# Kernel tuning notes

Hardware: AMD Instinct MI355X
Metric: run time of the kernel (lower is better)

## Reference

```python
import jax, jax.numpy as jnp
import numpy as np

N_HEAD = 16
N_KV_HEAD = 8
HEAD_DIM = 64
EPS_NORM = 1e-6


def _rms_norm(x):
    # F.rms_norm without learned weight
    return x * jax.lax.rsqrt(jnp.mean(x * x, axis=-1, keepdims=True) + EPS_NORM)


def _apply_rotary_emb(x, cos, sin):
    # x: [B, T, H, D]; cos/sin: [T, 1, D/2] (broadcast over B and H)
    d = x.shape[-1] // 2
    x1, x2 = x[..., :d], x[..., d:]
    return jnp.concatenate([x1 * cos + x2 * sin, -x1 * sin + x2 * cos], axis=-1)


def setup_inputs() -> dict:
    key = jax.random.key(0)
    ks = jax.random.split(key, 8)
    B, T, C = 2, 2048, 1024
    return {
        "x": jax.random.normal(ks[0], (B, T, C), jnp.float32),
        "cos": jax.random.uniform(ks[1], (T, 1, HEAD_DIM // 2), jnp.float32),
        "sin": jax.random.uniform(ks[2], (T, 1, HEAD_DIM // 2), jnp.float32),
        "Wq": jax.random.normal(ks[3], (N_HEAD * HEAD_DIM, C), jnp.float32) * 0.02,
        "Wk": jax.random.normal(ks[4], (N_KV_HEAD * HEAD_DIM, C), jnp.float32) * 0.02,
        "Wv": jax.random.normal(ks[5], (N_KV_HEAD * HEAD_DIM, C), jnp.float32) * 0.02,
        "Wproj": jax.random.normal(ks[6], (C, C), jnp.float32) * 0.02,
        "w_braid": jax.random.normal(ks[7], (HEAD_DIM,), jnp.float32),
    }


def reference(x, cos, sin, Wq, Wk, Wv, Wproj, w_braid):
    B, T, C = x.shape
    q = (x @ Wq.T).reshape(B, T, N_HEAD, HEAD_DIM)
    k = (x @ Wk.T).reshape(B, T, N_KV_HEAD, HEAD_DIM)
    v = (x @ Wv.T).reshape(B, T, N_KV_HEAD, HEAD_DIM)
    q = _rms_norm(_apply_rotary_emb(q, cos, sin))
    k = _rms_norm(_apply_rotary_emb(k, cos, sin))
    # [B, H, T, D]
    q = q.transpose(0, 2, 1, 3)
    k = k.transpose(0, 2, 1, 3)
    v = v.transpose(0, 2, 1, 3)
    rep = N_HEAD // N_KV_HEAD
    k = jnp.repeat(k, rep, axis=1)  # GQA repeat_kv_heads
    v = jnp.repeat(v, rep, axis=1)
    # rank-1 outer-sum score: s_q[i] + s_k[j]
    s_q = jnp.einsum("bhtd,d->bht", q, w_braid)
    s_k = jnp.einsum("bhsd,d->bhs", k, w_braid)
    scores = s_q[..., :, None] + s_k[..., None, :]  # [B, H, T, T]
    causal = jnp.arange(T)[:, None] >= jnp.arange(T)[None, :]
    scores = jnp.where(causal, scores, -jnp.inf)
    attn = jax.nn.sigmoid(scores)  # non-softmax gating
    y = jnp.einsum("bhts,bhsd->bhtd", attn, v)
    y = y / (T ** 0.5 + 1e-6)
    y = y.transpose(0, 2, 1, 3).reshape(B, T, C)
    return y @ Wproj.T
```

## Files before the change

### kernel.cpp

```cpp
#include <hip/hip_runtime.h>

#define BATCH   2
#define T_LEN   2048
#define C_DIM   1024
#define NH      16
#define NKV     8
#define HD      64

typedef unsigned short u16;
typedef __attribute__((ext_vector_type(8))) short short8;
typedef __attribute__((ext_vector_type(4))) float floatx4;

__device__ __forceinline__ u16 f2bf(float f) {
    union { float f; unsigned u; } v; v.f = f;
    unsigned r = v.u + 0x7FFF + ((v.u >> 16) & 1);
    return (u16)(r >> 16);
}

__device__ __forceinline__ void gload_lds16(const u16* g, u16* l) {
    __builtin_amdgcn_global_load_lds(
        (const __attribute__((address_space(1))) void*)g,
        (__attribute__((address_space(3))) void*)l, 16, 0, 0);
}

#define SBAR   __builtin_amdgcn_s_barrier()
#define SCHED0 __builtin_amdgcn_sched_barrier(0)
#define WAIT_LGKM0 asm volatile("s_waitcnt lgkmcnt(0)" ::: "memory")

__global__ __launch_bounds__(256)
void cvt_all(const float* __restrict__ x, const float* __restrict__ Wq,
             const float* __restrict__ Wk, const float* __restrict__ Wv,
             const float* __restrict__ Wp, u16* __restrict__ xb,
             u16* __restrict__ Wqkvb, u16* __restrict__ Wpb) {
    const int blk = blockIdx.x;
    const float* src; u16* dst; long off;
    if (blk < 4096)      { src = x;  dst = xb;              off = (long)blk * 1024; }
    else if (blk < 5120) { src = Wq; dst = Wqkvb;           off = (long)(blk - 4096) * 1024; }
    else if (blk < 5632) { src = Wk; dst = Wqkvb + 1048576; off = (long)(blk - 5120) * 1024; }
    else if (blk < 6144) { src = Wv; dst = Wqkvb + 1572864; off = (long)(blk - 5632) * 1024; }
    else                 { src = Wp; dst = Wpb;             off = (long)(blk - 6144) * 1024; }
    const long i = off + (long)threadIdx.x * 4;
    const float4 f = *(const float4*)&src[i];
    ushort4 o;
    o.x = f2bf(f.x); o.y = f2bf(f.y); o.z = f2bf(f.z); o.w = f2bf(f.w);
    *(ushort4*)&dst[i] = o;
}

__global__ __launch_bounds__(256)
void gemm_qkv(const u16* __restrict__ A, const u16* __restrict__ B,
              u16* __restrict__ Vt, float* __restrict__ esq,
              float* __restrict__ esk, const float* __restrict__ cosb,
              const float* __restrict__ sinb, const float* __restrict__ wb) {
    const int K  = 1024;
    const int NK = 16;
    __shared__ u16 As[2][128 * 64];
    __shared__ u16 Bs[2][128 * 64];
    const int tid    = threadIdx.x;
    const int lane   = tid & 63;
    const int wave   = tid >> 6;
    const int row_in = lane & 15;
    const int quad   = lane >> 4;
    const int rw     = (wave & 1) * 64;
    const int cw     = (wave >> 1) * 64;
    const int bi   = blockIdx.x;
    const int xcd  = bi & 7;
    const int bj   = bi >> 3;
    const int row0 = (bj >> 1) * 128;
    const int col0 = (xcd * 2 + (bj & 1)) * 128;

    floatx4 acc[4][4] = {};

    const int n    = row_in;
    const int xa   = n & 7;

    const int sl_r[4]  = { (0*256+tid)>>3, (1*256+tid)>>3, (2*256+tid)>>3, (3*256+tid)>>3 };
    const int sl_kc[4] = { ((0*256+tid)&7)^(sl_r[0]&7), ((1*256+tid)&7)^(sl_r[1]&7),
                           ((2*256+tid)&7)^(sl_r[2]&7), ((3*256+tid)&7)^(sl_r[3]&7) };

    #pragma unroll
    for (int c = 0; c < 4; ++c) {
        const int l = c * 256 + tid;
        gload_lds16(A + (size_t)(row0 + sl_r[c]) * K + 0  + sl_kc[c] * 8, &As[0][(size_t)l * 8]);
        gload_lds16(B + (size_t)(col0 + sl_r[c]) * K + 0  + sl_kc[c] * 8, &Bs[0][(size_t)l * 8]);
    }
    #pragma unroll
    for (int c = 0; c < 4; ++c) {
        const int l = c * 256 + tid;
        gload_lds16(A + (size_t)(row0 + sl_r[c]) * K + 64 + sl_kc[c] * 8, &As[1][(size_t)l * 8]);
        gload_lds16(B + (size_t)(col0 + sl_r[c]) * K + 64 + sl_kc[c] * 8, &Bs[1][(size_t)l * 8]);
    }
    asm volatile("s_waitcnt vmcnt(8)" ::: "memory");
    SBAR;
    SCHED0;

    int cur = 0;
    for (int kt = 0; kt < NK; ++kt) {
        short8 af[2][4], bf_[2][4];
        #pragma unroll
        for (int kk = 0; kk < 2; ++kk) {
            const int co = ((kk * 4 + quad) ^ xa) * 8;
            #pragma unroll
            for (int i = 0; i < 4; ++i)
                af[kk][i] = *(const short8*)&As[cur][(rw + 16 * i + n) * 64 + co];
            #pragma unroll
            for (int j = 0; j < 4; ++j)
                bf_[kk][j] = *(const short8*)&Bs[cur][(cw + 16 * j + n) * 64 + co];
        }
        WAIT_LGKM0;
        SCHED0;
        SBAR;
        SCHED0;

        if (kt + 2 < NK) {
            const int kn = (kt + 2) * 64;
            #pragma unroll
            for (int c = 0; c < 4; ++c) {
                const int l = c * 256 + tid;
                gload_lds16(A + (size_t)(row0 + sl_r[c]) * K + kn + sl_kc[c] * 8, &As[cur][(size_t)l * 8]);
                gload_lds16(B + (size_t)(col0 + sl_r[c]) * K + kn + sl_kc[c] * 8, &Bs[cur][(size_t)l * 8]);
            }
        }

        #pragma unroll
        for (int kk = 0; kk < 2; ++kk)
            #pragma unroll
            for (int i = 0; i < 4; ++i)
                #pragma unroll
                for (int j = 0; j < 4; ++j)
                    acc[i][j] = __builtin_amdgcn_mfma_f32_16x16x32_bf16(af[kk][i], bf_[kk][j], acc[i][j], 0, 0, 0);

        if (kt < NK - 2) { asm volatile("s_waitcnt vmcnt(8)" ::: "memory"); }
        else             { asm volatile("s_waitcnt vmcnt(0)" ::: "memory"); }
        SBAR;
        SCHED0;
        cur ^= 1;
    }

    const int cw_g = col0 + cw;
    const int rw_g = row0 + rw;
    const int ch   = cw_g >> 6;

    if (ch < 24) {
        const float w0 = wb[n], w1 = wb[16 + n], w2 = wb[32 + n], w3 = wb[48 + n];
        #pragma unroll
        for (int i = 0; i < 4; ++i)
            #pragma unroll
            for (int r = 0; r < 4; ++r) {
                const int grow = rw_g + 16 * i + quad * 4 + r;
                const int t = grow & 2047;
                const int b = grow >> 11;
                const float c0 = cosb[t * 32 + n];
                const float c1 = cosb[t * 32 + 16 + n];
                const float s0 = sinb[t * 32 + n];
                const float s1 = sinb[t * 32 + 16 + n];
                const float x0 = acc[i][0][r], x1 = acc[i][1][r];
                const float x2 = acc[i][2][r], x3 = acc[i][3][r];
                const float r0 = fmaf(x0, c0,  x2 * s0);
                const float r1 = fmaf(x1, c1,  x3 * s1);
                const float r2 = fmaf(x2, c0, -x0 * s0);
                const float r3 = fmaf(x3, c1, -x1 * s1);
                float ss = r0 * r0 + r1 * r1 + r2 * r2 + r3 * r3;
                float dt = r0 * w0 + r1 * w1 + r2 * w2 + r3 * w3;
                #pragma unroll
                for (int m = 1; m < 16; m <<= 1) {
                    ss += __shfl_xor(ss, m, 64);
                    dt += __shfl_xor(dt, m, 64);
                }
                const float val = dt * rsqrtf(ss * (1.0f / 64.0f) + 1e-6f);
                const float e = __expf(-fminf(fmaxf(val, -44.0f), 44.0f));
                if (n == 0) {
                    if (ch < 16) esq[((size_t)b * NH + ch) * T_LEN + t] = e;
                    else         esk[((size_t)b * NKV + ch - 16) * T_LEN + t] = e;
                }
            }
    } else {
        const int vcol = cw_g - 1536;
        const int b    = rw_g >> 11;
        const int tb   = (rw_g & 2047) + quad * 4;
        #pragma unroll
        for (int j = 0; j < 4; ++j) {
            const int dg  = vcol + 16 * j + n;
            const int kvh = dg >> 6;
            const int din = dg & 63;
            u16* dstp = Vt + ((size_t)(b * NKV + kvh) * 64 + din) * T_LEN;
            #pragma unroll
            for (int i = 0; i < 4; ++i) {
                ushort4 o;
                o.x = f2bf(acc[i][j][0]);
                o.y = f2bf(acc[i][j][1]);
                o.z = f2bf(acc[i][j][2]);
                o.w = f2bf(acc[i][j][3]);
                *(ushort4*)&dstp[tb + 16 * i] = o;
            }
        }
    }
}

__global__ __launch_bounds__(512)
void braid_attn(const float* __restrict__ esq, const float* __restrict__ esk,
                const u16* __restrict__ Vt, u16* __restrict__ yb) {
    __shared__ u16 Vd[2][2][4096];
    __shared__ float eskl[2][128];
    __shared__ float red[4096];

    const int bi   = blockIdx.x;
    const int g    = (bi & 7) * 2 + ((bi >> 8) & 1);
    const int wnd  = (bi >> 3) & 31;
    const int b    = g >> 3;
    const int kvh  = g & 7;
    const int h    = kvh * 2 + (wnd >> 4);
    const int p    = wnd & 15;
    const int bh   = b * 16 + h;
    const int tid  = threadIdx.x;
    const int lane = tid & 63;
    const int wave = tid >> 6;
    const int sg   = wave >> 2;
    const int w4   = wave & 3;
    const int n    = lane & 15;
    const int quad = lane >> 4;
    const int row  = w4 * 16 + n;

    const float* esq_p = esq + (size_t)bh * T_LEN;
    const float* esk_p = esk + ((size_t)b * NKV + kvh) * T_LEN;
    const u16*   vt_b  = Vt + ((size_t)b * NKV + kvh) * 64 * T_LEN;
    const float  inv   = (float)(1.0 / (45.254833995939045 + 1e-6));

    const int st_r  = tid >> 3;
    const int st_so = ((tid & 7) ^ (st_r & 7)) << 3;

    for (int ph = 0; ph < 2; ++ph) {
        const int t0 = (ph ? p : (31 - p)) * 64;
        const float a = esq_p[t0 + row];
        const int send = t0 + 64;
        floatx4 acc[4] = {};

        gload_lds16(vt_b + (size_t)st_r * T_LEN + st_so, &Vd[0][0][(size_t)tid * 8]);
        if (64 < send)
            gload_lds16(vt_b + (size_t)st_r * T_LEN + 64 + st_so, &Vd[0][1][(size_t)tid * 8]);
        if (tid < 128 && (tid < 64 || 64 < send))
            eskl[0][tid] = esk_p[tid];
        __syncthreads();

        int cur = 0;
        for (int s0 = 0; s0 < send; s0 += 128) {
            const int s0n = s0 + 128;
            if (s0n < send) {
                gload_lds16(vt_b + (size_t)st_r * T_LEN + s0n + st_so, &Vd[cur ^ 1][0][(size_t)tid * 8]);
                if (s0n + 64 < send)
                    gload_lds16(vt_b + (size_t)st_r * T_LEN + s0n + 64 + st_so, &Vd[cur ^ 1][1][(size_t)tid * 8]);
                if (tid < 128 && (tid < 64 || s0n + 64 < send))
                    eskl[cur ^ 1][tid] = esk_p[s0n + tid];
            }

            const int s0g = s0 + sg * 64;
            if (s0g < send) {
                const bool diag = (s0g == t0);
                #pragma unroll
                for (int kk = 0; kk < 2; ++kk) {
                    const float* eb = &eskl[cur][sg * 64 + kk * 32 + quad * 8];
                    const float4 e0 = *(const float4*)eb;
                    const float4 e1 = *(const float4*)(eb + 4);
                    const float ev[8] = {e0.x, e0.y, e0.z, e0.w, e1.x, e1.y, e1.z, e1.w};
                    union { unsigned u[4]; short8 s8; } af;
                    #pragma unroll
                    for (int jj = 0; jj < 4; ++jj) {
                        float r0 = __builtin_amdgcn_rcpf(fmaf(ev[2 * jj],     a, 1.0f));
                        float r1 = __builtin_amdgcn_rcpf(fmaf(ev[2 * jj + 1], a, 1.0f));
                        if (diag) {
                            const int s_ = kk * 32 + quad * 8 + 2 * jj;
                            if (s_     > row) r0 = 0.0f;
                            if (s_ + 1 > row) r1 = 0.0f;
                        }
                        af.u[jj] = __builtin_amdgcn_perm(__float_as_uint(r1),
                                                         __float_as_uint(r0), 0x07060302u);
                    }
                    #pragma unroll
                    for (int j = 0; j < 4; ++j) {
                        const short8 bfr = *(const short8*)
                            &Vd[cur][sg][(16 * j + n) * 64 + (((kk * 4 + quad) ^ (n & 7)) << 3)];
                        acc[j] = __builtin_amdgcn_mfma_f32_16x16x32_bf16(af.s8, bfr, acc[j], 0, 0, 0);
                    }
                }
            }
            __syncthreads();
            cur ^= 1;
        }

        if (sg == 1) {
            #pragma unroll
            for (int j = 0; j < 4; ++j)
                #pragma unroll
                for (int r = 0; r < 4; ++r)
                    red[(j * 4 + r) * 256 + w4 * 64 + lane] = acc[j][r];
        }
        __syncthreads();
        if (sg == 0) {
            #pragma unroll
            for (int j = 0; j < 4; ++j)
                #pragma unroll
                for (int r = 0; r < 4; ++r) {
                    const float o = acc[j][r] + red[(j * 4 + r) * 256 + w4 * 64 + lane];
                    const int t = t0 + w4 * 16 + quad * 4 + r;
                    yb[((size_t)b * T_LEN + t) * C_DIM + h * HD + 16 * j + n] = f2bf(o * inv);
                }
        }
    }
}

__global__ __launch_bounds__(256)
void gemm_proj(const u16* __restrict__ A, const u16* __restrict__ B,
               float* __restrict__ C, int M, int N, int K) {
    const int NK = 16;
    __shared__ u16 As[2][128 * 64];
    __shared__ u16 Bs[2][64 * 64];
    const int tid    = threadIdx.x;
    const int lane   = tid & 63;
    const int wave   = tid >> 6;
    const int row_in = lane & 15;
    const int quad   = lane >> 4;
    const int rw     = (wave & 1) * 64;
    const int cw     = (wave >> 1) * 32;
    const int bi   = blockIdx.x;
    const int xcd  = bi & 7;
    const int bj   = bi >> 3;
    const int row0 = (bj >> 1) * 128;
    const int col0 = (xcd * 2 + (bj & 1)) * 64;

    floatx4 acc[4][2] = {};

    const int n  = row_in;
    const int xa = n & 7;

    const int sa_r[4]  = { (0*256+tid)>>3, (1*256+tid)>>3, (2*256+tid)>>3, (3*256+tid)>>3 };
    const int sa_kc[4] = { ((0*256+tid)&7)^(sa_r[0]&7), ((1*256+tid)&7)^(sa_r[1]&7),
                           ((2*256+tid)&7)^(sa_r[2]&7), ((3*256+tid)&7)^(sa_r[3]&7) };
    const int sb_r[2]  = { (0*256+tid)>>3, (1*256+tid)>>3 };
    const int sb_kc[2] = { ((0*256+tid)&7)^(sb_r[0]&7), ((1*256+tid)&7)^(sb_r[1]&7) };

    #pragma unroll
    for (int c = 0; c < 4; ++c)
        gload_lds16(A + (size_t)(row0 + sa_r[c]) * K + 0 + sa_kc[c] * 8, &As[0][(size_t)(c*256+tid) * 8]);
    #pragma unroll
    for (int c = 0; c < 2; ++c)
        gload_lds16(B + (size_t)(col0 + sb_r[c]) * K + 0 + sb_kc[c] * 8, &Bs[0][(size_t)(c*256+tid) * 8]);
    #pragma unroll
    for (int c = 0; c < 4; ++c)
        gload_lds16(A + (size_t)(row0 + sa_r[c]) * K + 64 + sa_kc[c] * 8, &As[1][(size_t)(c*256+tid) * 8]);
    #pragma unroll
    for (int c = 0; c < 2; ++c)
        gload_lds16(B + (size_t)(col0 + sb_r[c]) * K + 64 + sb_kc[c] * 8, &Bs[1][(size_t)(c*256+tid) * 8]);
    asm volatile("s_waitcnt vmcnt(6)" ::: "memory");
    SBAR;
    SCHED0;

    int cur = 0;
    for (int kt = 0; kt < NK; ++kt) {
        short8 af[2][4], bf_[2][2];
        #pragma unroll
        for (int kk = 0; kk < 2; ++kk) {
            const int co = ((kk * 4 + quad) ^ xa) * 8;
            #pragma unroll
            for (int i = 0; i < 4; ++i)
                af[kk][i] = *(const short8*)&As[cur][(rw + 16 * i + n) * 64 + co];
            #pragma unroll
            for (int j = 0; j < 2; ++j)
                bf_[kk][j] = *(const short8*)&Bs[cur][(cw + 16 * j + n) * 64 + co];
        }
        WAIT_LGKM0;
        SCHED0;
        SBAR;
        SCHED0;

        if (kt + 2 < NK) {
            const int kn = (kt + 2) * 64;
            #pragma unroll
            for (int c = 0; c < 4; ++c)
                gload_lds16(A + (size_t)(row0 + sa_r[c]) * K + kn + sa_kc[c] * 8, &As[cur][(size_t)(c*256+tid) * 8]);
            #pragma unroll
            for (int c = 0; c < 2; ++c)
                gload_lds16(B + (size_t)(col0 + sb_r[c]) * K + kn + sb_kc[c] * 8, &Bs[cur][(size_t)(c*256+tid) * 8]);
        }

        #pragma unroll
        for (int kk = 0; kk < 2; ++kk)
            #pragma unroll
            for (int i = 0; i < 4; ++i)
                #pragma unroll
                for (int j = 0; j < 2; ++j)
                    acc[i][j] = __builtin_amdgcn_mfma_f32_16x16x32_bf16(af[kk][i], bf_[kk][j], acc[i][j], 0, 0, 0);

        if (kt < NK - 2) { asm volatile("s_waitcnt vmcnt(6)" ::: "memory"); }
        else             { asm volatile("s_waitcnt vmcnt(0)" ::: "memory"); }
        SBAR;
        SCHED0;
        cur ^= 1;
    }

    #pragma unroll
    for (int i = 0; i < 4; ++i)
        #pragma unroll
        for (int j = 0; j < 2; ++j)
            #pragma unroll
            for (int r = 0; r < 4; ++r)
                C[(size_t)(row0 + rw + 16 * i + quad * 4 + r) * N + col0 + cw + 16 * j + row_in]
                    = acc[i][j][r];
}

extern "C" void kernel_launch(void* const* d_in, const int* in_sizes, int n_in,
                              void* d_out, int out_size, void* d_ws, size_t ws_size,
                              hipStream_t stream) {
    const float* x     = (const float*)d_in[0];
    const float* cosb  = (const float*)d_in[1];
    const float* sinb  = (const float*)d_in[2];
    const float* Wq    = (const float*)d_in[3];
    const float* Wk    = (const float*)d_in[4];
    const float* Wv    = (const float*)d_in[5];
    const float* Wproj = (const float*)d_in[6];
    const float* wb    = (const float*)d_in[7];
    float* out = (float*)d_out;

    char* w = (char*)d_ws;
    u16* xb     = (u16*)w;  w += (size_t)4096 * 1024 * 2;
    u16* Wqkvb  = (u16*)w;  w += (size_t)2048 * 1024 * 2;
    u16* Wpb    = (u16*)w;  w += (size_t)1024 * 1024 * 2;
    u16* yb     = (u16*)w;  w += (size_t)4096 * 1024 * 2;
    u16* VtB    = (u16*)w;  w += (size_t)BATCH * NKV * 64 * T_LEN * 2;
    float* esq  = (float*)w; w += (size_t)BATCH * NH * T_LEN * 4;
    float* esk  = (float*)w; w += (size_t)BATCH * NKV * T_LEN * 4;

    dim3 blk(256);
    cvt_all<<<7168, blk, 0, stream>>>(x, Wq, Wk, Wv, Wproj, xb, Wqkvb, Wpb);
    gemm_qkv<<<512, blk, 0, stream>>>(xb, Wqkvb, VtB, esq, esk, cosb, sinb, wb);
    braid_attn<<<512, dim3(512), 0, stream>>>(esq, esk, VtB, yb);
    gemm_proj<<<512, blk, 0, stream>>>(yb, Wpb, out, 4096, 1024, 1024);
}
```

Before: 148.0 us.

## Fuse all stages into one persistent kernel with grid barriers

Replaces the four separate launches (convert, QKV GEMM, attention, projection GEMM) with a single persistent kernel of 512 blocks that runs each stage in turn, separated by atomic-counter grid barriers and sharing LDS through a union. The aim is to remove kernel launch gaps and tail idle time between stages. In exchange, the attention stage is rewritten for 256 threads instead of 512. The barriers rely on all 512 blocks being co-resident (launch bounds of 2 blocks per CU) and use a timeout spin, which could silently break correctness if residency fails.

```diff
diff --git a/kernel.cpp b/kernel.cpp
--- a/kernel.cpp
+++ b/kernel.cpp
@@ -6,6 +6,7 @@
 #define NH      16
 #define NKV     8
 #define HD      64
+#define NBLK    512
 
 typedef unsigned short u16;
 typedef __attribute__((ext_vector_type(8))) short short8;
@@ -27,237 +28,271 @@
 #define SCHED0 __builtin_amdgcn_sched_barrier(0)
 #define WAIT_LGKM0 asm volatile("s_waitcnt lgkmcnt(0)" ::: "memory")
 
-__global__ __launch_bounds__(256)
-void cvt_all(const float* __restrict__ x, const float* __restrict__ Wq,
-             const float* __restrict__ Wk, const float* __restrict__ Wv,
-             const float* __restrict__ Wp, u16* __restrict__ xb,
-             u16* __restrict__ Wqkvb, u16* __restrict__ Wpb) {
-    const int blk = blockIdx.x;
-    const float* src; u16* dst; long off;
-    if (blk < 4096)      { src = x;  dst = xb;              off = (long)blk * 1024; }
-    else if (blk < 5120) { src = Wq; dst = Wqkvb;           off = (long)(blk - 4096) * 1024; }
-    else if (blk < 5632) { src = Wk; dst = Wqkvb + 1048576; off = (long)(blk - 5120) * 1024; }
-    else if (blk < 6144) { src = Wv; dst = Wqkvb + 1572864; off = (long)(blk - 5632) * 1024; }
-    else                 { src = Wp; dst = Wpb;             off = (long)(blk - 6144) * 1024; }
-    const long i = off + (long)threadIdx.x * 4;
-    const float4 f = *(const float4*)&src[i];
-    ushort4 o;
-    o.x = f2bf(f.x); o.y = f2bf(f.y); o.z = f2bf(f.z); o.w = f2bf(f.w);
-    *(ushort4*)&dst[i] = o;
-}
-
-__global__ __launch_bounds__(256)
-void gemm_qkv(const u16* __restrict__ A, const u16* __restrict__ B,
-              u16* __restrict__ Vt, float* __restrict__ esq,
-              float* __restrict__ esk, const float* __restrict__ cosb,
-              const float* __restrict__ sinb, const float* __restrict__ wb) {
-    const int K  = 1024;
-    const int NK = 16;
-    __shared__ u16 As[2][128 * 64];
-    __shared__ u16 Bs[2][128 * 64];
-    const int tid    = threadIdx.x;
-    const int lane   = tid & 63;
-    const int wave   = tid >> 6;
-    const int row_in = lane & 15;
-    const int quad   = lane >> 4;
-    const int rw     = (wave & 1) * 64;
-    const int cw     = (wave >> 1) * 64;
-    const int bi   = blockIdx.x;
-    const int xcd  = bi & 7;
-    const int bj   = bi >> 3;
-    const int row0 = (bj >> 1) * 128;
-    const int col0 = (xcd * 2 + (bj & 1)) * 128;
-
-    floatx4 acc[4][4] = {};
-
-    const int n    = row_in;
-    const int xa   = n & 7;
-
-    const int sl_r[4]  = { (0*256+tid)>>3, (1*256+tid)>>3, (2*256+tid)>>3, (3*256+tid)>>3 };
-    const int sl_kc[4] = { ((0*256+tid)&7)^(sl_r[0]&7), ((1*256+tid)&7)^(sl_r[1]&7),
-                           ((2*256+tid)&7)^(sl_r[2]&7), ((3*256+tid)&7)^(sl_r[3]&7) };
-
-    #pragma unroll
-    for (int c = 0; c < 4; ++c) {
-        const int l = c * 256 + tid;
-        gload_lds16(A + (size_t)(row0 + sl_r[c]) * K + 0  + sl_kc[c] * 8, &As[0][(size_t)l * 8]);
-        gload_lds16(B + (size_t)(col0 + sl_r[c]) * K + 0  + sl_kc[c] * 8, &Bs[0][(size_t)l * 8]);
+__device__ __forceinline__ void grid_barrier(unsigned* bar, int idx) {
+    __syncthreads();
+    if (threadIdx.x == 0) {
+        __threadfence();
+        unsigned* cnt = bar + idx * 64;
+        __hip_atomic_fetch_add(cnt, 1u, __ATOMIC_ACQ_REL, __HIP_MEMORY_SCOPE_AGENT);
+        const long long lim = 5000000LL;
+        long long t0 = (long long)__builtin_amdgcn_s_memrealtime();
+        while (__hip_atomic_load(cnt, __ATOMIC_ACQUIRE, __HIP_MEMORY_SCOPE_AGENT) < (unsigned)NBLK) {
+            if ((long long)__builtin_amdgcn_s_memrealtime() - t0 > lim) break;
+        }
+        __threadfence();
     }
-    #pragma unroll
-    for (int c = 0; c < 4; ++c) {
-        const int l = c * 256 + tid;
-        gload_lds16(A + (size_t)(row0 + sl_r[c]) * K + 64 + sl_kc[c] * 8, &As[1][(size_t)l * 8]);
-        gload_lds16(B + (size_t)(col0 + sl_r[c]) * K + 64 + sl_kc[c] * 8, &Bs[1][(size_t)l * 8]);
+    __syncthreads();
+}
+
+__global__ __launch_bounds__(64)
+void bar_init(unsigned* bar) {
+    bar[threadIdx.x * 4] = 0;
+    bar[threadIdx.x * 4 + 1] = 0;
+    bar[threadIdx.x * 4 + 2] = 0;
+    bar[threadIdx.x * 4 + 3] = 0;
+}
+
+struct SMg { u16 As[2][128 * 64]; u16 Bs[2][128 * 64]; };
+struct SMp { u16 As[2][128 * 64]; u16 Bs[2][64 * 64]; };
+struct SMa { u16 Vd[2][4096]; float eskl[2][64]; };
+union __align__(16) SMu { SMg g; SMp p; SMa a; };
+
+__global__ __launch_bounds__(256, 2)
+void fused_all(const float* __restrict__ x, const float* __restrict__ cosb,
+               const float* __restrict__ sinb, const float* __restrict__ Wq,
+               const float* __restrict__ Wk, const float* __restrict__ Wv,
+               const float* __restrict__ Wp, const float* __restrict__ wb,
+               u16* __restrict__ xb, u16* __restrict__ Wqkvb,
+               u16* __restrict__ Wpb, u16* __restrict__ yb,
+               u16* __restrict__ VtB, float* __restrict__ esq,
+               float* __restrict__ esk, float* __restrict__ out,
+               unsigned* __restrict__ bar) {
+    __shared__ SMu sm;
+
+    {
+        const int tid = threadIdx.x;
+        #pragma unroll
+        for (int i = 0; i < 14; ++i) {
+            const int blk = blockIdx.x * 14 + i;
+            const float* src; u16* dst; long off;
+            if (blk < 4096)      { src = x;  dst = xb;              off = (long)blk * 1024; }
+            else if (blk < 5120) { src = Wq; dst = Wqkvb;           off = (long)(blk - 4096) * 1024; }
+            else if (blk < 5632) { src = Wk; dst = Wqkvb + 1048576; off = (long)(blk - 5120) * 1024; }
+            else if (blk < 6144) { src = Wv; dst = Wqkvb + 1572864; off = (long)(blk - 5632) * 1024; }
+            else                 { src = Wp; dst = Wpb;             off = (long)(blk - 6144) * 1024; }
+            const long idx = off + (long)tid * 4;
+            const float4 f = *(const float4*)&src[idx];
+            ushort4 o;
+            o.x = f2bf(f.x); o.y = f2bf(f.y); o.z = f2bf(f.z); o.w = f2bf(f.w);
+            *(ushort4*)&dst[idx] = o;
+        }
     }
-    asm volatile("s_waitcnt vmcnt(8)" ::: "memory");
-    SBAR;
-    SCHED0;
-
-    int cur = 0;
-    for (int kt = 0; kt < NK; ++kt) {
-        short8 af[2][4], bf_[2][4];
-        #pragma unroll
-        for (int kk = 0; kk < 2; ++kk) {
-            const int co = ((kk * 4 + quad) ^ xa) * 8;
-            #pragma unroll
-            for (int i = 0; i < 4; ++i)
-                af[kk][i] = *(const short8*)&As[cur][(rw + 16 * i + n) * 64 + co];
-            #pragma unroll
-            for (int j = 0; j < 4; ++j)
-                bf_[kk][j] = *(const short8*)&Bs[cur][(cw + 16 * j + n) * 64 + co];
-        }
-        WAIT_LGKM0;
-        SCHED0;
+    grid_barrier(bar, 0);
+
+    {
+        const u16* A = xb;
+        const u16* B = Wqkvb;
+        const int K  = 1024;
+        const int NK = 16;
+        u16 (&As)[2][128 * 64] = sm.g.As;
+        u16 (&Bs)[2][128 * 64] = sm.g.Bs;
+        const int tid    = threadIdx.x;
+        const int lane   = tid & 63;
+        const int wave   = tid >> 6;
+        const int row_in = lane & 15;
+        const int quad   = lane >> 4;
+        const int rw     = (wave & 1) * 64;
+        const int cw     = (wave >> 1) * 64;
+        const int bi   = blockIdx.x;
+        const int xcd  = bi & 7;
+        const int bj   = bi >> 3;
+        const int row0 = (bj >> 1) * 128;
+        const int col0 = (xcd * 2 + (bj & 1)) * 128;
+
+        floatx4 acc[4][4] = {};
+        const int n  = row_in;
+        const int xa = n & 7;
+
+        const int sl_r[4]  = { (0*256+tid)>>3, (1*256+tid)>>3, (2*256+tid)>>3, (3*256+tid)>>3 };
+        const int sl_kc[4] = { ((0*256+tid)&7)^(sl_r[0]&7), ((1*256+tid)&7)^(sl_r[1]&7),
+                               ((2*256+tid)&7)^(sl_r[2]&7), ((3*256+tid)&7)^(sl_r[3]&7) };
+
+        #pragma unroll
+        for (int c = 0; c < 4; ++c) {
+            const int l = c * 256 + tid;
+            gload_lds16(A + (size_t)(row0 + sl_r[c]) * K + 0  + sl_kc[c] * 8, &As[0][(size_t)l * 8]);
+            gload_lds16(B + (size_t)(col0 + sl_r[c]) * K + 0  + sl_kc[c] * 8, &Bs[0][(size_t)l * 8]);
+        }
+        #pragma unroll
+        for (int c = 0; c < 4; ++c) {
+            const int l = c * 256 + tid;
+            gload_lds16(A + (size_t)(row0 + sl_r[c]) * K + 64 + sl_kc[c] * 8, &As[1][(size_t)l * 8]);
+            gload_lds16(B + (size_t)(col0 + sl_r[c]) * K + 64 + sl_kc[c] * 8, &Bs[1][(size_t)l * 8]);
+        }
+        asm volatile("s_waitcnt vmcnt(8)" ::: "memory");
         SBAR;
         SCHED0;
 
-        if (kt + 2 < NK) {
-            const int kn = (kt + 2) * 64;
-            #pragma unroll
-            for (int c = 0; c < 4; ++c) {
-                const int l = c * 256 + tid;
-                gload_lds16(A + (size_t)(row0 + sl_r[c]) * K + kn + sl_kc[c] * 8, &As[cur][(size_t)l * 8]);
-                gload_lds16(B + (size_t)(col0 + sl_r[c]) * K + kn + sl_kc[c] * 8, &Bs[cur][(size_t)l * 8]);
-            }
-        }
-
-        #pragma unroll
-        for (int kk = 0; kk < 2; ++kk)
+        int cur = 0;
+        for (int kt = 0; kt < NK; ++kt) {
+            short8 af[2][4], bf_[2][4];
+            #pragma unroll
+            for (int kk = 0; kk < 2; ++kk) {
+                const int co = ((kk * 4 + quad) ^ xa) * 8;
+                #pragma unroll
+                for (int i = 0; i < 4; ++i)
+                    af[kk][i] = *(const short8*)&As[cur][(rw + 16 * i + n) * 64 + co];
+                #pragma unroll
+                for (int j = 0; j < 4; ++j)
+                    bf_[kk][j] = *(const short8*)&Bs[cur][(cw + 16 * j + n) * 64 + co];
+            }
+            WAIT_LGKM0;
+            SCHED0;
+            SBAR;
+            SCHED0;
+
+            if (kt + 2 < NK) {
+                const int kn = (kt + 2) * 64;
+                #pragma unroll
+                for (int c = 0; c < 4; ++c) {
+                    const int l = c * 256 + tid;
+                    gload_lds16(A + (size_t)(row0 + sl_r[c]) * K + kn + sl_kc[c] * 8, &As[cur][(size_t)l * 8]);
+                    gload_lds16(B + (size_t)(col0 + sl_r[c]) * K + kn + sl_kc[c] * 8, &Bs[cur][(size_t)l * 8]);
+                }
+            }
+
+            #pragma unroll
+            for (int kk = 0; kk < 2; ++kk)
+                #pragma unroll
+                for (int i = 0; i < 4; ++i)
+                    #pragma unroll
+                    for (int j = 0; j < 4; ++j)
+                        acc[i][j] = __builtin_amdgcn_mfma_f32_16x16x32_bf16(af[kk][i], bf_[kk][j], acc[i][j], 0, 0, 0);
+
+            if (kt < NK - 2) { asm volatile("s_waitcnt vmcnt(8)" ::: "memory"); }
+            else             { asm volatile("s_waitcnt vmcnt(0)" ::: "memory"); }
+            SBAR;
+            SCHED0;
+            cur ^= 1;
+        }
+
+        const int cw_g = col0 + cw;
+        const int rw_g = row0 + rw;
+        const int ch   = cw_g >> 6;
+
+        if (ch < 24) {
+            const float w0 = wb[n], w1 = wb[16 + n], w2 = wb[32 + n], w3 = wb[48 + n];
             #pragma unroll
             for (int i = 0; i < 4; ++i)
                 #pragma unroll
-                for (int j = 0; j < 4; ++j)
-                    acc[i][j] = __builtin_amdgcn_mfma_f32_16x16x32_bf16(af[kk][i], bf_[kk][j], acc[i][j], 0, 0, 0);
-
-        if (kt < NK - 2) { asm volatile("s_waitcnt vmcnt(8)" ::: "memory"); }
-        else             { asm volatile("s_waitcnt vmcnt(0)" ::: "memory"); }
-        SBAR;
-        SCHED0;
-        cur ^= 1;
+                for (int r = 0; r < 4; ++r) {
+                    const int grow = rw_g + 16 * i + quad * 4 + r;
+                    const int t = grow & 2047;
+                    const int b = grow >> 11;
+                    const float c0 = cosb[t * 32 + n];
+                    const float c1 = cosb[t * 32 + 16 + n];
+                    const float s0 = sinb[t * 32 + n];
+                    const float s1 = sinb[t * 32 + 16 + n];
+                    const float x0 = acc[i][0][r], x1 = acc[i][1][r];
+                    const float x2 = acc[i][2][r], x3 = acc[i][3][r];
+                    const float r0 = fmaf(x0, c0,  x2 * s0);
+                    const float r1 = fmaf(x1, c1,  x3 * s1);
+                    const float r2 = fmaf(x2, c0, -x0 * s0);
+                    const float r3 = fmaf(x3, c1, -x1 * s1);
+                    float ss = r0 * r0 + r1 * r1 + r2 * r2 + r3 * r3;
+                    float dt = r0 * w0 + r1 * w1 + r2 * w2 + r3 * w3;
+                    #pragma unroll
+                    for (int m = 1; m < 16; m <<= 1) {
+                        ss += __shfl_xor(ss, m, 64);
+                        dt += __shfl_xor(dt, m, 64);
+                    }
+                    const float val = dt * rsqrtf(ss * (1.0f / 64.0f) + 1e-6f);
+                    const float e = __expf(-fminf(fmaxf(val, -44.0f), 44.0f));
+                    if (n == 0) {
+                        if (ch < 16) esq[((size_t)b * NH + ch) * T_LEN + t] = e;
+                        else         esk[((size_t)b * NKV + ch - 16) * T_LEN + t] = e;
+                    }
+                }
+        } else {
+            const int vcol = cw_g - 1536;
+            const int b    = rw_g >> 11;
+            const int tb   = (rw_g & 2047) + quad * 4;
+            #pragma unroll
+            for (int j = 0; j < 4; ++j) {
+                const int dg  = vcol + 16 * j + n;
+                const int kvh = dg >> 6;
+                const int din = dg & 63;
+                u16* dstp = VtB + ((size_t)(b * NKV + kvh) * 64 + din) * T_LEN;
+                #pragma unroll
+                for (int i = 0; i < 4; ++i) {
+                    ushort4 o;
+                    o.x = f2bf(acc[i][j][0]);
+                    o.y = f2bf(acc[i][j][1]);
+                    o.z = f2bf(acc[i][j][2]);
+                    o.w = f2bf(acc[i][j][3]);
+                    *(ushort4*)&dstp[tb + 16 * i] = o;
+                }
+            }
+        }
     }
-
-    const int cw_g = col0 + cw;
-    const int rw_g = row0 + rw;
-    const int ch   = cw_g >> 6;
-
-    if (ch < 24) {
-        const float w0 = wb[n], w1 = wb[16 + n], w2 = wb[32 + n], w3 = wb[48 + n];
-        #pragma unroll
-        for (int i = 0; i < 4; ++i)
-            #pragma unroll
-            for (int r = 0; r < 4; ++r) {
-                const int grow = rw_g + 16 * i + quad * 4 + r;
-                const int t = grow & 2047;
-                const int b = grow >> 11;
-                const float c0 = cosb[t * 32 + n];
-                const float c1 = cosb[t * 32 + 16 + n];
-                const float s0 = sinb[t * 32 + n];
-                const float s1 = sinb[t * 32 + 16 + n];
-                const float x0 = acc[i][0][r], x1 = acc[i][1][r];
-                const float x2 = acc[i][2][r], x3 = acc[i][3][r];
-                const float r0 = fmaf(x0, c0,  x2 * s0);
-                const float r1 = fmaf(x1, c1,  x3 * s1);
-                const float r2 = fmaf(x2, c0, -x0 * s0);
-                const float r3 = fmaf(x3, c1, -x1 * s1);
-                float ss = r0 * r0 + r1 * r1 + r2 * r2 + r3 * r3;
-                float dt = r0 * w0 + r1 * w1 + r2 * w2 + r3 * w3;
-                #pragma unroll
-                for (int m = 1; m < 16; m <<= 1) {
-                    ss += __shfl_xor(ss, m, 64);
-                    dt += __shfl_xor(dt, m, 64);
-                }
-                const float val = dt * rsqrtf(ss * (1.0f / 64.0f) + 1e-6f);
-                const float e = __expf(-fminf(fmaxf(val, -44.0f), 44.0f));
-                if (n == 0) {
-                    if (ch < 16) esq[((size_t)b * NH + ch) * T_LEN + t] = e;
-                    else         esk[((size_t)b * NKV + ch - 16) * T_LEN + t] = e;
-                }
-            }
-    } else {
-        const int vcol = cw_g - 1536;
-        const int b    = rw_g >> 11;
-        const int tb   = (rw_g & 2047) + quad * 4;
-        #pragma unroll
-        for (int j = 0; j < 4; ++j) {
-            const int dg  = vcol + 16 * j + n;
-            const int kvh = dg >> 6;
-            const int din = dg & 63;
-            u16* dstp = Vt + ((size_t)(b * NKV + kvh) * 64 + din) * T_LEN;
-            #pragma unroll
-            for (int i = 0; i < 4; ++i) {
-                ushort4 o;
-                o.x = f2bf(acc[i][j][0]);
-                o.y = f2bf(acc[i][j][1]);
-                o.z = f2bf(acc[i][j][2]);
-                o.w = f2bf(acc[i][j][3]);
-                *(ushort4*)&dstp[tb + 16 * i] = o;
-            }
-        }
-    }
-}
-
-__global__ __launch_bounds__(512)
-void braid_attn(const float* __restrict__ esq, const float* __restrict__ esk,
-                const u16* __restrict__ Vt, u16* __restrict__ yb) {
-    __shared__ u16 Vd[2][2][4096];
-    __shared__ float eskl[2][128];
-    __shared__ float red[4096];
-
-    const int bi   = blockIdx.x;
-    const int g    = (bi & 7) * 2 + ((bi >> 8) & 1);
-    const int wnd  = (bi >> 3) & 31;
-    const int b    = g >> 3;
-    const int kvh  = g & 7;
-    const int h    = kvh * 2 + (wnd >> 4);
-    const int p    = wnd & 15;
-    const int bh   = b * 16 + h;
-    const int tid  = threadIdx.x;
-    const int lane = tid & 63;
-    const int wave = tid >> 6;
-    const int sg   = wave >> 2;
-    const int w4   = wave & 3;
-    const int n    = lane & 15;
-    const int quad = lane >> 4;
-    const int row  = w4 * 16 + n;
-
-    const float* esq_p = esq + (size_t)bh * T_LEN;
-    const float* esk_p = esk + ((size_t)b * NKV + kvh) * T_LEN;
-    const u16*   vt_b  = Vt + ((size_t)b * NKV + kvh) * 64 * T_LEN;
-    const float  inv   = (float)(1.0 / (45.254833995939045 + 1e-6));
-
-    const int st_r  = tid >> 3;
-    const int st_so = ((tid & 7) ^ (st_r & 7)) << 3;
-
-    for (int ph = 0; ph < 2; ++ph) {
-        const int t0 = (ph ? p : (31 - p)) * 64;
-        const float a = esq_p[t0 + row];
-        const int send = t0 + 64;
-        floatx4 acc[4] = {};
-
-        gload_lds16(vt_b + (size_t)st_r * T_LEN + st_so, &Vd[0][0][(size_t)tid * 8]);
-        if (64 < send)
-            gload_lds16(vt_b + (size_t)st_r * T_LEN + 64 + st_so, &Vd[0][1][(size_t)tid * 8]);
-        if (tid < 128 && (tid < 64 || 64 < send))
-            eskl[0][tid] = esk_p[tid];
-        __syncthreads();
-
-        int cur = 0;
-        for (int s0 = 0; s0 < send; s0 += 128) {
-            const int s0n = s0 + 128;
-            if (s0n < send) {
-                gload_lds16(vt_b + (size_t)st_r * T_LEN + s0n + st_so, &Vd[cur ^ 1][0][(size_t)tid * 8]);
-                if (s0n + 64 < send)
-                    gload_lds16(vt_b + (size_t)st_r * T_LEN + s0n + 64 + st_so, &Vd[cur ^ 1][1][(size_t)tid * 8]);
-                if (tid < 128 && (tid < 64 || s0n + 64 < send))
-                    eskl[cur ^ 1][tid] = esk_p[s0n + tid];
-            }
-
-            const int s0g = s0 + sg * 64;
-            if (s0g < send) {
-                const bool diag = (s0g == t0);
+    grid_barrier(bar, 1);
+
+    {
+        u16   (&Vd)[2][4096] = sm.a.Vd;
+        float (&eskl)[2][64] = sm.a.eskl;
+
+        const int bi   = blockIdx.x;
+        const int g    = (bi & 7) * 2 + ((bi >> 8) & 1);
+        const int wnd  = (bi >> 3) & 31;
+        const int b    = g >> 3;
+        const int kvh  = g & 7;
+        const int h    = kvh * 2 + (wnd >> 4);
+        const int p    = wnd & 15;
+        const int bh   = b * 16 + h;
+        const int tid  = threadIdx.x;
+        const int lane = tid & 63;
+        const int w4   = tid >> 6;
+        const int n    = lane & 15;
+        const int quad = lane >> 4;
+        const int row  = w4 * 16 + n;
+
+        const float* esq_p = esq + (size_t)bh * T_LEN;
+        const float* esk_p = esk + ((size_t)b * NKV + kvh) * T_LEN;
+        const u16*   vt_b  = VtB + ((size_t)b * NKV + kvh) * 64 * T_LEN;
+        const float  inv   = (float)(1.0 / (45.254833995939045 + 1e-6));
+
+        const int st_r[2]  = { (0*256+tid)>>3, (1*256+tid)>>3 };
+        const int st_so[2] = { (((0*256+tid)&7) ^ (st_r[0]&7)) << 3,
+                               (((1*256+tid)&7) ^ (st_r[1]&7)) << 3 };
+
+        for (int ph = 0; ph < 2; ++ph) {
+            const int t0 = (ph ? p : (31 - p)) * 64;
+            const float a = esq_p[t0 + row];
+            const int send = t0 + 64;
+            floatx4 acc[4] = {};
+
+            #pragma unroll
+            for (int c = 0; c < 2; ++c)
+                gload_lds16(vt_b + (size_t)st_r[c] * T_LEN + st_so[c],
+                            &Vd[0][(size_t)(c * 256 + tid) * 8]);
+            if (tid < 64) eskl[0][tid] = esk_p[tid];
+            __syncthreads();
+
+            int cur = 0;
+            for (int s0 = 0; s0 < send; s0 += 64) {
+                const int s0n = s0 + 64;
+                if (s0n < send) {
+                    #pragma unroll
+                    for (int c = 0; c < 2; ++c)
+                        gload_lds16(vt_b + (size_t)st_r[c] * T_LEN + s0n + st_so[c],
+                                    &Vd[cur ^ 1][(size_t)(c * 256 + tid) * 8]);
+                    if (tid < 64) eskl[cur ^ 1][tid] = esk_p[s0n + tid];
+                }
+
+                const bool diag = (s0 == t0);
                 #pragma unroll
                 for (int kk = 0; kk < 2; ++kk) {
-                    const float* eb = &eskl[cur][sg * 64 + kk * 32 + quad * 8];
+                    const float* eb = &eskl[cur][kk * 32 + quad * 8];
                     const float4 e0 = *(const float4*)eb;
                     const float4 e1 = *(const float4*)(eb + 4);
                     const float ev[8] = {e0.x, e0.y, e0.z, e0.w, e1.x, e1.y, e1.z, e1.w};
@@ -277,133 +312,126 @@
                     #pragma unroll
                     for (int j = 0; j < 4; ++j) {
                         const short8 bfr = *(const short8*)
-                            &Vd[cur][sg][(16 * j + n) * 64 + (((kk * 4 + quad) ^ (n & 7)) << 3)];
+                            &Vd[cur][(16 * j + n) * 64 + (((kk * 4 + quad) ^ (n & 7)) << 3)];
                         acc[j] = __builtin_amdgcn_mfma_f32_16x16x32_bf16(af.s8, bfr, acc[j], 0, 0, 0);
                     }
                 }
-            }
-            __syncthreads();
-            cur ^= 1;
-        }
-
-        if (sg == 1) {
+                __syncthreads();
+                cur ^= 1;
+            }
+
             #pragma unroll
             for (int j = 0; j < 4; ++j)
                 #pragma unroll
-                for (int r = 0; r < 4; ++r)
-                    red[(j * 4 + r) * 256 + w4 * 64 + lane] = acc[j][r];
-        }
-        __syncthreads();
-        if (sg == 0) {
-            #pragma unroll
-            for (int j = 0; j < 4; ++j)
-                #pragma unroll
                 for (int r = 0; r < 4; ++r) {
-                    const float o = acc[j][r] + red[(j * 4 + r) * 256 + w4 * 64 + lane];
                     const int t = t0 + w4 * 16 + quad * 4 + r;
-                    yb[((size_t)b * T_LEN + t) * C_DIM + h * HD + 16 * j + n] = f2bf(o * inv);
+                    yb[((size_t)b * T_LEN + t) * C_DIM + h * HD + 16 * j + n]
+                        = f2bf(acc[j][r] * inv);
                 }
         }
     }
-}
-
-__global__ __launch_bounds__(256)
-void gemm_proj(const u16* __restrict__ A, const u16* __restrict__ B,
-               float* __restrict__ C, int M, int N, int K) {
-    const int NK = 16;
-    __shared__ u16 As[2][128 * 64];
-    __shared__ u16 Bs[2][64 * 64];
-    const int tid    = threadIdx.x;
-    const int lane   = tid & 63;
-    const int wave   = tid >> 6;
-    const int row_in = lane & 15;
-    const int quad   = lane >> 4;
-    const int rw     = (wave & 1) * 64;
-    const int cw     = (wave >> 1) * 32;
-    const int bi   = blockIdx.x;
-    const int xcd  = bi & 7;
-    const int bj   = bi >> 3;
-    const int row0 = (bj >> 1) * 128;
-    const int col0 = (xcd * 2 + (bj & 1)) * 64;
-
-    floatx4 acc[4][2] = {};
-
-    const int n  = row_in;
-    const int xa = n & 7;
-
-    const int sa_r[4]  = { (0*256+tid)>>3, (1*256+tid)>>3, (2*256+tid)>>3, (3*256+tid)>>3 };
-    const int sa_kc[4] = { ((0*256+tid)&7)^(sa_r[0]&7), ((1*256+tid)&7)^(sa_r[1]&7),
-                           ((2*256+tid)&7)^(sa_r[2]&7), ((3*256+tid)&7)^(sa_r[3]&7) };
-    const int sb_r[2]  = { (0*256+tid)>>3, (1*256+tid)>>3 };
-    const int sb_kc[2] = { ((0*256+tid)&7)^(sb_r[0]&7), ((1*256+tid)&7)^(sb_r[1]&7) };
-
-    #pragma unroll
-    for (int c = 0; c < 4; ++c)
-        gload_lds16(A + (size_t)(row0 + sa_r[c]) * K + 0 + sa_kc[c] * 8, &As[0][(size_t)(c*256+tid) * 8]);
-    #pragma unroll
-    for (int c = 0; c < 2; ++c)
-        gload_lds16(B + (size_t)(col0 + sb_r[c]) * K + 0 + sb_kc[c] * 8, &Bs[0][(size_t)(c*256+tid) * 8]);
-    #pragma unroll
-    for (int c = 0; c < 4; ++c)
-        gload_lds16(A + (size_t)(row0 + sa_r[c]) * K + 64 + sa_kc[c] * 8, &As[1][(size_t)(c*256+tid) * 8]);
-    #pragma unroll
-    for (int c = 0; c < 2; ++c)
-        gload_lds16(B + (size_t)(col0 + sb_r[c]) * K + 64 + sb_kc[c] * 8, &Bs[1][(size_t)(c*256+tid) * 8]);
-    asm volatile("s_waitcnt vmcnt(6)" ::: "memory");
-    SBAR;
-    SCHED0;
-
-    int cur = 0;
-    for (int kt = 0; kt < NK; ++kt) {
-        short8 af[2][4], bf_[2][2];
-        #pragma unroll
-        for (int kk = 0; kk < 2; ++kk) {
-            const int co = ((kk * 4 + quad) ^ xa) * 8;
-            #pragma unroll
-            for (int i = 0; i < 4; ++i)
-                af[kk][i] = *(const short8*)&As[cur][(rw + 16 * i + n) * 64 + co];
-            #pragma unroll
-            for (int j = 0; j < 2; ++j)
-                bf_[kk][j] = *(const short8*)&Bs[cur][(cw + 16 * j + n) * 64 + co];
-        }
-        WAIT_LGKM0;
-        SCHED0;
+    grid_barrier(bar, 2);
+
+    {
+        const u16* A = yb;
+        const u16* B = Wpb;
+        float* C = out;
+        const int K  = 1024;
+        const int N  = 1024;
+        const int NK = 16;
+        u16 (&As)[2][128 * 64] = sm.p.As;
+        u16 (&Bs)[2][64 * 64]  = sm.p.Bs;
+        const int tid    = threadIdx.x;
+        const int lane   = tid & 63;
+        const int wave   = tid >> 6;
+        const int row_in = lane & 15;
+        const int quad   = lane >> 4;
+        const int rw     = (wave & 1) * 64;
+        const int cw     = (wave >> 1) * 32;
+        const int bi   = blockIdx.x;
+        const int xcd  = bi & 7;
+        const int bj   = bi >> 3;
+        const int row0 = (bj >> 1) * 128;
+        const int col0 = (xcd * 2 + (bj & 1)) * 64;
+
+        floatx4 acc[4][2] = {};
+        const int n  = row_in;
+        const int xa = n & 7;
+
+        const int sa_r[4]  = { (0*256+tid)>>3, (1*256+tid)>>3, (2*256+tid)>>3, (3*256+tid)>>3 };
+        const int sa_kc[4] = { ((0*256+tid)&7)^(sa_r[0]&7), ((1*256+tid)&7)^(sa_r[1]&7),
+                               ((2*256+tid)&7)^(sa_r[2]&7), ((3*256+tid)&7)^(sa_r[3]&7) };
+        const int sb_r[2]  = { (0*256+tid)>>3, (1*256+tid)>>3 };
+        const int sb_kc[2] = { ((0*256+tid)&7)^(sb_r[0]&7), ((1*256+tid)&7)^(sb_r[1]&7) };
+
+        #pragma unroll
+        for (int c = 0; c < 4; ++c)
+            gload_lds16(A + (size_t)(row0 + sa_r[c]) * K + 0 + sa_kc[c] * 8, &As[0][(size_t)(c*256+tid) * 8]);
+        #pragma unroll
+        for (int c = 0; c < 2; ++c)
+            gload_lds16(B + (size_t)(col0 + sb_r[c]) * K + 0 + sb_kc[c] * 8, &Bs[0][(size_t)(c*256+tid) * 8]);
+        #pragma unroll
+        for (int c = 0; c < 4; ++c)
+            gload_lds16(A + (size_t)(row0 + sa_r[c]) * K + 64 + sa_kc[c] * 8, &As[1][(size_t)(c*256+tid) * 8]);
+        #pragma unroll
+        for (int c = 0; c < 2; ++c)
+            gload_lds16(B + (size_t)(col0 + sb_r[c]) * K + 64 + sb_kc[c] * 8, &Bs[1][(size_t)(c*256+tid) * 8]);
+        asm volatile("s_waitcnt vmcnt(6)" ::: "memory");
         SBAR;
         SCHED0;
 
-        if (kt + 2 < NK) {
-            const int kn = (kt + 2) * 64;
-            #pragma unroll
-            for (int c = 0; c < 4; ++c)
-                gload_lds16(A + (size_t)(row0 + sa_r[c]) * K + kn + sa_kc[c] * 8, &As[cur][(size_t)(c*256+tid) * 8]);
-            #pragma unroll
-            for (int c = 0; c < 2; ++c)
-                gload_lds16(B + (size_t)(col0 + sb_r[c]) * K + kn + sb_kc[c] * 8, &Bs[cur][(size_t)(c*256+tid) * 8]);
-        }
-
-        #pragma unroll
-        for (int kk = 0; kk < 2; ++kk)
-            #pragma unroll
-            for (int i = 0; i < 4; ++i)
+        int cur = 0;
+        for (int kt = 0; kt < NK; ++kt) {
+            short8 af[2][4], bf_[2][2];
+            #pragma unroll
+            for (int kk = 0; kk < 2; ++kk) {
+                const int co = ((kk * 4 + quad) ^ xa) * 8;
+                #pragma unroll
+                for (int i = 0; i < 4; ++i)
+                    af[kk][i] = *(const short8*)&As[cur][(rw + 16 * i + n) * 64 + co];
                 #pragma unroll
                 for (int j = 0; j < 2; ++j)
-                    acc[i][j] = __builtin_amdgcn_mfma_f32_16x16x32_bf16(af[kk][i], bf_[kk][j], acc[i][j], 0, 0, 0);
-
-        if (kt < NK - 2) { asm volatile("s_waitcnt vmcnt(6)" ::: "memory"); }
-        else             { asm volatile("s_waitcnt vmcnt(0)" ::: "memory"); }
-        SBAR;
-        SCHED0;
-        cur ^= 1;
+                    bf_[kk][j] = *(const short8*)&Bs[cur][(cw + 16 * j + n) * 64 + co];
+            }
+            WAIT_LGKM0;
+            SCHED0;
+            SBAR;
+            SCHED0;
+
+            if (kt + 2 < NK) {
+                const int kn = (kt + 2) * 64;
+                #pragma unroll
+                for (int c = 0; c < 4; ++c)
+                    gload_lds16(A + (size_t)(row0 + sa_r[c]) * K + kn + sa_kc[c] * 8, &As[cur][(size_t)(c*256+tid) * 8]);
+                #pragma unroll
+                for (int c = 0; c < 2; ++c)
+                    gload_lds16(B + (size_t)(col0 + sb_r[c]) * K + kn + sb_kc[c] * 8, &Bs[cur][(size_t)(c*256+tid) * 8]);
+            }
+
+            #pragma unroll
+            for (int kk = 0; kk < 2; ++kk)
+                #pragma unroll
+                for (int i = 0; i < 4; ++i)
+                    #pragma unroll
+                    for (int j = 0; j < 2; ++j)
+                        acc[i][j] = __builtin_amdgcn_mfma_f32_16x16x32_bf16(af[kk][i], bf_[kk][j], acc[i][j], 0, 0, 0);
+
+            if (kt < NK - 2) { asm volatile("s_waitcnt vmcnt(6)" ::: "memory"); }
+            else             { asm volatile("s_waitcnt vmcnt(0)" ::: "memory"); }
+            SBAR;
+            SCHED0;
+            cur ^= 1;
+        }
+
+        #pragma unroll
+        for (int i = 0; i < 4; ++i)
+            #pragma unroll
+            for (int j = 0; j < 2; ++j)
+                #pragma unroll
+                for (int r = 0; r < 4; ++r)
+                    C[(size_t)(row0 + rw + 16 * i + quad * 4 + r) * N + col0 + cw + 16 * j + row_in]
+                        = acc[i][j][r];
     }
-
-    #pragma unroll
-    for (int i = 0; i < 4; ++i)
-        #pragma unroll
-        for (int j = 0; j < 2; ++j)
-            #pragma unroll
-            for (int r = 0; r < 4; ++r)
-                C[(size_t)(row0 + rw + 16 * i + quad * 4 + r) * N + col0 + cw + 16 * j + row_in]
-                    = acc[i][j][r];
 }
 
 extern "C" void kernel_launch(void* const* d_in, const int* in_sizes, int n_in,
@@ -427,10 +455,10 @@
     u16* VtB    = (u16*)w;  w += (size_t)BATCH * NKV * 64 * T_LEN * 2;
     float* esq  = (float*)w; w += (size_t)BATCH * NH * T_LEN * 4;
     float* esk  = (float*)w; w += (size_t)BATCH * NKV * T_LEN * 4;
-
-    dim3 blk(256);
-    cvt_all<<<7168, blk, 0, stream>>>(x, Wq, Wk, Wv, Wproj, xb, Wqkvb, Wpb);
-    gemm_qkv<<<512, blk, 0, stream>>>(xb, Wqkvb, VtB, esq, esk, cosb, sinb, wb);
-    braid_attn<<<512, dim3(512), 0, stream>>>(esq, esk, VtB, yb);
-    gemm_proj<<<512, blk, 0, stream>>>(yb, Wpb, out, 4096, 1024, 1024);
-}
+    unsigned* bar = (unsigned*)w; w += 4096;
+
+    bar_init<<<1, 64, 0, stream>>>(bar);
+    fused_all<<<NBLK, dim3(256), 0, stream>>>(
+        x, cosb, sinb, Wq, Wk, Wv, Wproj, wb,
+        xb, Wqkvb, Wpb, yb, VtB, esq, esk, out, bar);
+}
```

Measured after the change: 379.1 us. 2.56x slower.

## Load V and key scores directly from global memory, dropping LDS staging

Applied to the files above, without the earlier changes.

The attention kernel no longer stages V tiles and the exp-key-score vector through double-buffered shared memory with async global-to-LDS loads and per-iteration barriers. Each wave instead reads its MFMA B operands and key scores straight from global memory, relying on the L1/L2 caches. This removes the LDS traffic and the barriers inside the loop, and the two wave groups now walk their own key ranges independently. In exchange, global loads are no longer shared across waves and their latency is not hidden by explicit prefetch.

```diff
diff --git a/kernel.cpp b/kernel.cpp
--- a/kernel.cpp
+++ b/kernel.cpp
@@ -199,8 +199,6 @@
 __global__ __launch_bounds__(512)
 void braid_attn(const float* __restrict__ esq, const float* __restrict__ esk,
                 const u16* __restrict__ Vt, u16* __restrict__ yb) {
-    __shared__ u16 Vd[2][2][4096];
-    __shared__ float eskl[2][128];
     __shared__ float red[4096];
 
     const int bi   = blockIdx.x;
@@ -225,8 +223,9 @@
     const u16*   vt_b  = Vt + ((size_t)b * NKV + kvh) * 64 * T_LEN;
     const float  inv   = (float)(1.0 / (45.254833995939045 + 1e-6));
 
-    const int st_r  = tid >> 3;
-    const int st_so = ((tid & 7) ^ (st_r & 7)) << 3;
+    const u16* vrow[4];
+    #pragma unroll
+    for (int j = 0; j < 4; ++j) vrow[j] = vt_b + (size_t)(16 * j + n) * T_LEN;
 
     for (int ph = 0; ph < 2; ++ph) {
         const int t0 = (ph ? p : (31 - p)) * 64;
@@ -234,58 +233,36 @@
         const int send = t0 + 64;
         floatx4 acc[4] = {};
 
-        gload_lds16(vt_b + (size_t)st_r * T_LEN + st_so, &Vd[0][0][(size_t)tid * 8]);
-        if (64 < send)
-            gload_lds16(vt_b + (size_t)st_r * T_LEN + 64 + st_so, &Vd[0][1][(size_t)tid * 8]);
-        if (tid < 128 && (tid < 64 || 64 < send))
-            eskl[0][tid] = esk_p[tid];
-        __syncthreads();
-
-        int cur = 0;
-        for (int s0 = 0; s0 < send; s0 += 128) {
-            const int s0n = s0 + 128;
-            if (s0n < send) {
-                gload_lds16(vt_b + (size_t)st_r * T_LEN + s0n + st_so, &Vd[cur ^ 1][0][(size_t)tid * 8]);
-                if (s0n + 64 < send)
-                    gload_lds16(vt_b + (size_t)st_r * T_LEN + s0n + 64 + st_so, &Vd[cur ^ 1][1][(size_t)tid * 8]);
-                if (tid < 128 && (tid < 64 || s0n + 64 < send))
-                    eskl[cur ^ 1][tid] = esk_p[s0n + tid];
-            }
-
-            const int s0g = s0 + sg * 64;
-            if (s0g < send) {
-                const bool diag = (s0g == t0);
-                #pragma unroll
-                for (int kk = 0; kk < 2; ++kk) {
-                    const float* eb = &eskl[cur][sg * 64 + kk * 32 + quad * 8];
-                    const float4 e0 = *(const float4*)eb;
-                    const float4 e1 = *(const float4*)(eb + 4);
-                    const float ev[8] = {e0.x, e0.y, e0.z, e0.w, e1.x, e1.y, e1.z, e1.w};
-                    union { unsigned u[4]; short8 s8; } af;
-                    #pragma unroll
-                    for (int jj = 0; jj < 4; ++jj) {
-                        float r0 = __builtin_amdgcn_rcpf(fmaf(ev[2 * jj],     a, 1.0f));
-                        float r1 = __builtin_amdgcn_rcpf(fmaf(ev[2 * jj + 1], a, 1.0f));
-                        if (diag) {
-                            const int s_ = kk * 32 + quad * 8 + 2 * jj;
-                            if (s_     > row) r0 = 0.0f;
-                            if (s_ + 1 > row) r1 = 0.0f;
-                        }
-                        af.u[jj] = __builtin_amdgcn_perm(__float_as_uint(r1),
-                                                         __float_as_uint(r0), 0x07060302u);
+        for (int s0g = sg * 64; s0g < send; s0g += 128) {
+            const bool diag = (s0g == t0);
+            #pragma unroll
+            for (int kk = 0; kk < 2; ++kk) {
+                const int co = s0g + kk * 32 + quad * 8;
+                const float4 e0 = *(const float4*)&esk_p[co];
+                const float4 e1 = *(const float4*)&esk_p[co + 4];
+                const float ev[8] = {e0.x, e0.y, e0.z, e0.w, e1.x, e1.y, e1.z, e1.w};
+                union { unsigned u[4]; short8 s8; } af;
+                #pragma unroll
+                for (int jj = 0; jj < 4; ++jj) {
+                    float r0 = __builtin_amdgcn_rcpf(fmaf(ev[2 * jj],     a, 1.0f));
+                    float r1 = __builtin_amdgcn_rcpf(fmaf(ev[2 * jj + 1], a, 1.0f));
+                    if (diag) {
+                        const int s_ = kk * 32 + quad * 8 + 2 * jj;
+                        if (s_     > row) r0 = 0.0f;
+                        if (s_ + 1 > row) r1 = 0.0f;
                     }
-                    #pragma unroll
-                    for (int j = 0; j < 4; ++j) {
-                        const short8 bfr = *(const short8*)
-                            &Vd[cur][sg][(16 * j + n) * 64 + (((kk * 4 + quad) ^ (n & 7)) << 3)];
-                        acc[j] = __builtin_amdgcn_mfma_f32_16x16x32_bf16(af.s8, bfr, acc[j], 0, 0, 0);
-                    }
+                    af.u[jj] = __builtin_amdgcn_perm(__float_as_uint(r1),
+                                                     __float_as_uint(r0), 0x07060302u);
+                }
+                #pragma unroll
+                for (int j = 0; j < 4; ++j) {
+                    const short8 bfr = *(const short8*)&vrow[j][co];
+                    acc[j] = __builtin_amdgcn_mfma_f32_16x16x32_bf16(af.s8, bfr, acc[j], 0, 0, 0);
                 }
             }
-            __syncthreads();
-            cur ^= 1;
-        }
-
+        }
+
+        __syncthreads();
         if (sg == 1) {
             #pragma unroll
             for (int j = 0; j < 4; ++j)
```

Measured after the change: 193.8 us. 30.9% more time.
